# Kernel tuning notes

Hardware: AMD Instinct MI355X
Metric: run time of the kernel (lower is better)

## Reference

```python
import jax, jax.numpy as jnp
import numpy as np

N_CHARS, EMB, HID, SEQ = 256, 512, 2048, 4096

def setup_inputs() -> dict:
    key = jax.random.key(0)
    ks = jax.random.split(key, 13)
    s = lambda k, shape: jax.random.normal(k, shape, dtype=jnp.float32) * 0.02
    return {
        "input_seq": jax.random.randint(ks[0], (SEQ,), 0, N_CHARS, dtype=jnp.int32),
        "emb_table": s(ks[1], (N_CHARS, EMB)),
        "Wf": s(ks[2], (HID, EMB + HID)), "bf": s(ks[3], (HID,)),
        "Wi": s(ks[4], (HID, EMB + HID)), "bi": s(ks[5], (HID,)),
        "Wo": s(ks[6], (HID, EMB + HID)), "bo": s(ks[7], (HID,)),
        "Wc": s(ks[8], (HID, EMB + HID)), "bc": s(ks[9], (HID,)),
        "Wy": s(ks[10], (N_CHARS, HID)), "by": s(ks[11], (N_CHARS,)),
    }

def reference(input_seq, emb_table, Wf, bf, Wi, bi, Wo, bo, Wc, bc, Wy, by):
    E = emb_table.shape[1]
    embs = emb_table[input_seq]  # [T, E]
    # Split each gate Linear on concat([emb, h]) into input and recurrent parts.
    # Input contributions for all timesteps as one GEMM per gate: [T, H]
    xf = embs @ Wf[:, :E].T + bf
    xi = embs @ Wi[:, :E].T + bi
    xo = embs @ Wo[:, :E].T + bo
    xc = embs @ Wc[:, :E].T + bc
    Wfh, Wih, Woh, Wch = Wf[:, E:], Wi[:, E:], Wo[:, E:], Wc[:, E:]

    def step(carry, xs):
        h, c = carry
        xf_t, xi_t, xo_t, xc_t = xs
        ft = jax.nn.sigmoid(xf_t + Wfh @ h)
        it = jax.nn.sigmoid(xi_t + Wih @ h)
        tct = jnp.tanh(xc_t + Wch @ h)
        c_new = ft * c + it * tct
        ot = jax.nn.sigmoid(xo_t + Woh @ h)
        h_new = ot * jnp.tanh(c_new)
        o = Wy @ h_new + by
        return (h_new, c_new), o

    h0 = jnp.zeros((Wf.shape[0],), dtype=embs.dtype)
    c0 = jnp.zeros((Wf.shape[0],), dtype=embs.dtype)
    (h, c), outs = jax.lax.scan(step, (h0, c0), (xf, xi, xo, xc))
    return outs, h, c
```

## Files before the change

kernel.cpp:

```cpp
#include <hip/hip_runtime.h>
#include <hip/hip_fp16.h>

#define SEQL 4096
#define EMBD 512
#define HIDD 2048
#define NCH  256
#define WCOL 2560

typedef _Float16 half8_t __attribute__((ext_vector_type(8)));
typedef _Float16 half2_t __attribute__((ext_vector_type(2)));
typedef float    float4_t __attribute__((ext_vector_type(4)));

#if __has_builtin(__builtin_amdgcn_fdot2)
__device__ __forceinline__ float fdot2u(unsigned a, unsigned b, float c) {
  return __builtin_amdgcn_fdot2(__builtin_bit_cast(half2_t, a),
                                __builtin_bit_cast(half2_t, b), c, false);
}
#else
__device__ __forceinline__ float fdot2u(unsigned a, unsigned b, float c) {
  half2_t ha = __builtin_bit_cast(half2_t, a), hb = __builtin_bit_cast(half2_t, b);
  return c + (float)ha.x * (float)hb.x + (float)ha.y * (float)hb.y;
}
#endif

__device__ __forceinline__ float sigm_f(float x)  { return 1.f / (1.f + __expf(-x)); }
__device__ __forceinline__ float tanh_f(float x)  { return 1.f - 2.f / (__expf(2.f * x) + 1.f); }

__global__ void prep_kernel(const int* __restrict__ seq, const float* __restrict__ emb,
                            const float* __restrict__ Wf, const float* __restrict__ Wi,
                            const float* __restrict__ Wo, const float* __restrict__ Wc,
                            const float* __restrict__ Wy,
                            _Float16* __restrict__ emb16, _Float16* __restrict__ Wst16,
                            _Float16* __restrict__ Wy16, unsigned* __restrict__ hstage)
{
  const long nEmb = (long)SEQL * EMBD;
  const long nWst = (long)4 * HIDD * EMBD;
  const long nWy  = (long)NCH * HIDD;
  const long nHs  = 2 * HIDD;
  const long total = nEmb + nWst + nWy + nHs;
  long stride = (long)gridDim.x * blockDim.x;
  for (long i = (long)blockIdx.x * blockDim.x + threadIdx.x; i < total; i += stride) {
    if (i < nEmb) {
      long t = i >> 9, e = i & 511;
      emb16[i] = (_Float16)emb[(long)seq[t] * EMBD + e];
    } else if (i < nEmb + nWst) {
      long j = i - nEmb;
      long row = j >> 9, k = j & 511;
      long r = row >> 11, jr = row & 2047;
      const float* W = (r == 0) ? Wf : (r == 1) ? Wi : (r == 2) ? Wo : Wc;
      Wst16[j] = (_Float16)W[jr * WCOL + k];
    } else if (i < nEmb + nWst + nWy) {
      long j = i - nEmb - nWst;
      Wy16[j] = (_Float16)Wy[j];
    } else {
      hstage[i - nEmb - nWst - nWy] = 0u;
    }
  }
}

template<int K, int MODE>
__global__ __launch_bounds__(256) void gemm_bt(const _Float16* __restrict__ A,
                                               const _Float16* __restrict__ B,
                                               _Float16* __restrict__ C16,
                                               float* __restrict__ Cf,
                                               const float* __restrict__ bias, int N)
{
  __shared__ _Float16 At[128 * 32];
  __shared__ _Float16 Bt[128 * 32];
  const int tid = threadIdx.x;
  const int w = tid >> 6, lane = tid & 63;
  const int wm = w >> 1, wn = w & 1;
  const int lr = lane & 15, kg = lane >> 4;
  const long tm = (long)blockIdx.y * 128;
  const long tn = (long)blockIdx.x * 128;

  float4_t acc[4][4];
#pragma unroll
  for (int a = 0; a < 4; a++)
#pragma unroll
    for (int b = 0; b < 4; b++) acc[a][b] = (float4_t)0.f;

  for (int kt = 0; kt < K; kt += 32) {
    __syncthreads();
#pragma unroll
    for (int s = 0; s < 2; s++) {
      int l = s * 256 + tid;
      int row = l >> 2, ks = (l & 3) * 8;
      *(uint4*)&At[row * 32 + ks] = *(const uint4*)&A[(tm + row) * (long)K + kt + ks];
      *(uint4*)&Bt[row * 32 + ks] = *(const uint4*)&B[(tn + row) * (long)K + kt + ks];
    }
    __syncthreads();
    half8_t af[4], bf[4];
#pragma unroll
    for (int mi = 0; mi < 4; mi++) af[mi] = *(const half8_t*)&At[(wm * 64 + mi * 16 + lr) * 32 + kg * 8];
#pragma unroll
    for (int ni = 0; ni < 4; ni++) bf[ni] = *(const half8_t*)&Bt[(wn * 64 + ni * 16 + lr) * 32 + kg * 8];
#pragma unroll
    for (int mi = 0; mi < 4; mi++)
#pragma unroll
      for (int ni = 0; ni < 4; ni++)
        acc[mi][ni] = __builtin_amdgcn_mfma_f32_16x16x32_f16(af[mi], bf[ni], acc[mi][ni], 0, 0, 0);
  }

#pragma unroll
  for (int mi = 0; mi < 4; mi++)
#pragma unroll
    for (int ni = 0; ni < 4; ni++)
#pragma unroll
      for (int i = 0; i < 4; i++) {
        long gm = tm + wm * 64 + mi * 16 + kg * 4 + i;
        long gn = tn + wn * 64 + ni * 16 + lr;
        float v = acc[mi][ni][i];
        if (MODE == 0) C16[gm * (long)N + gn] = (_Float16)v;
        else           Cf[gm * (long)N + gn] = v + bias[gn];
      }
}

__global__ __launch_bounds__(512) void lstm_seq(
    const _Float16* __restrict__ xq,
    const float* __restrict__ Wf, const float* __restrict__ Wi,
    const float* __restrict__ Wo, const float* __restrict__ Wc,
    const float* __restrict__ bfp, const float* __restrict__ bip,
    const float* __restrict__ bop, const float* __restrict__ bcp,
    unsigned* __restrict__ hstage,
    _Float16* __restrict__ H16,
    float* __restrict__ out)
{
  __shared__ unsigned hbuf[HIDD / 2];
  __shared__ float gl[32];

  const int tid  = threadIdx.x;
  const int wave = tid >> 6, lane = tid & 63;
  const int rw   = lane >> 4, hsub = lane & 15;
  const int row_local = wave * 4 + rw;
  const int r  = row_local >> 3;
  const int jj = row_local & 7;
  const int g  = blockIdx.x;
  const int jg = g * 8 + jj;

  const float* Wsel = (r == 0) ? Wf : (r == 1) ? Wi : (r == 2) ? Wo : Wc;
  const float* bsel = (r == 0) ? bfp : (r == 1) ? bip : (r == 2) ? bop : bcp;
  const float* wrow = Wsel + (long)jg * WCOL + EMBD;

  uint2 wreg[32];
#pragma unroll
  for (int it = 0; it < 32; ++it) {
    const float4 wv = *(const float4*)(wrow + it * 64 + hsub * 4);
    half2_t lo = { (_Float16)wv.x, (_Float16)wv.y };
    half2_t hi = { (_Float16)wv.z, (_Float16)wv.w };
    wreg[it].x = __builtin_bit_cast(unsigned, lo);
    wreg[it].y = __builtin_bit_cast(unsigned, hi);
  }
  const float bias = (hsub == 0) ? bsel[jg] : 0.f;

  float c = 0.f;

  for (int t = 0; t < SEQL; ++t) {
    float xv = 0.f;
    if (hsub == 0) xv = (float)xq[(long)t * 8192 + r * HIDD + g * 8 + jj];

    if (t == 0) {
      hbuf[tid * 2] = 0u; hbuf[tid * 2 + 1] = 0u;
    } else {
      const int base = (t & 1) * HIDD + tid * 4;
      const unsigned tg = (unsigned)t;
      unsigned v0, v1, v2, v3; int guard = 0;
      for (;;) {
        v0 = __hip_atomic_load(&hstage[base + 0], __ATOMIC_RELAXED, __HIP_MEMORY_SCOPE_AGENT);
        v1 = __hip_atomic_load(&hstage[base + 1], __ATOMIC_RELAXED, __HIP_MEMORY_SCOPE_AGENT);
        v2 = __hip_atomic_load(&hstage[base + 2], __ATOMIC_RELAXED, __HIP_MEMORY_SCOPE_AGENT);
        v3 = __hip_atomic_load(&hstage[base + 3], __ATOMIC_RELAXED, __HIP_MEMORY_SCOPE_AGENT);
        if ((v0 >> 16) == tg && (v1 >> 16) == tg && (v2 >> 16) == tg && (v3 >> 16) == tg) break;
        if (++guard > (1 << 24)) break;
      }
      hbuf[tid * 2]     = (v0 & 0xffffu) | (v1 << 16);
      hbuf[tid * 2 + 1] = (v2 & 0xffffu) | (v3 << 16);
    }
    __syncthreads();

    float a0 = 0.f, a1 = 0.f, a2 = 0.f, a3 = 0.f;
#pragma unroll
    for (int it = 0; it < 32; ++it) {
      const uint2 hv = *(const uint2*)&hbuf[it * 32 + hsub * 2];
      if (it & 1) { a2 = fdot2u(wreg[it].x, hv.x, a2); a3 = fdot2u(wreg[it].y, hv.y, a3); }
      else        { a0 = fdot2u(wreg[it].x, hv.x, a0); a1 = fdot2u(wreg[it].y, hv.y, a1); }
    }
    float s = (a0 + a1) + (a2 + a3);
    s += __shfl_xor(s, 1, 64);
    s += __shfl_xor(s, 2, 64);
    s += __shfl_xor(s, 4, 64);
    s += __shfl_xor(s, 8, 64);

    if (hsub == 0) {
      const float pre = s + xv + bias;
      gl[row_local] = (r == 3) ? tanh_f(pre) : sigm_f(pre);
    }
    __syncthreads();

    if (tid < 8) {
      const float f  = gl[tid];
      const float ii = gl[8 + tid];
      const float o  = gl[16 + tid];
      const float cg = gl[24 + tid];
      c = f * c + ii * cg;
      const float h = o * tanh_f(c);
      const _Float16 hh = (_Float16)h;
      H16[(long)t * HIDD + g * 8 + tid] = hh;
      const unsigned pk = (unsigned)__builtin_bit_cast(unsigned short, hh) | ((unsigned)(t + 1) << 16);
      __hip_atomic_store(&hstage[((t + 1) & 1) * HIDD + g * 8 + tid], pk,
                         __ATOMIC_RELAXED, __HIP_MEMORY_SCOPE_AGENT);
      if (t == SEQL - 1) {
        out[(long)SEQL * NCH + g * 8 + tid] = h;
        out[(long)SEQL * NCH + HIDD + g * 8 + tid] = c;
      }
    }
  }
}

extern "C" void kernel_launch(void* const* d_in, const int* in_sizes, int n_in,
                              void* d_out, int out_size, void* d_ws, size_t ws_size,
                              hipStream_t stream) {
  const int*   seq = (const int*)d_in[0];
  const float* emb = (const float*)d_in[1];
  const float* Wf  = (const float*)d_in[2];
  const float* bf_ = (const float*)d_in[3];
  const float* Wi  = (const float*)d_in[4];
  const float* bi_ = (const float*)d_in[5];
  const float* Wo  = (const float*)d_in[6];
  const float* bo_ = (const float*)d_in[7];
  const float* Wc  = (const float*)d_in[8];
  const float* bc_ = (const float*)d_in[9];
  const float* Wy  = (const float*)d_in[10];
  const float* by  = (const float*)d_in[11];
  float* out = (float*)d_out;

  char* ws = (char*)d_ws;
  _Float16* xq     = (_Float16*)(ws);
  _Float16* emb16  = (_Float16*)(ws + (64ll << 20));
  _Float16* Wst16  = (_Float16*)(ws + (68ll << 20));
  _Float16* Wy16   = (_Float16*)(ws + (76ll << 20));
  _Float16* H16    = (_Float16*)(ws + (77ll << 20));
  unsigned* hstage = (unsigned*)(ws + (93ll << 20));

  prep_kernel<<<2048, 256, 0, stream>>>(seq, emb, Wf, Wi, Wo, Wc, Wy,
                                        emb16, Wst16, Wy16, hstage);

  dim3 g1(8192 / 128, 4096 / 128);
  gemm_bt<EMBD, 0><<<g1, 256, 0, stream>>>(emb16, Wst16, xq, nullptr, nullptr, 8192);

  lstm_seq<<<256, 512, 0, stream>>>(xq, Wf, Wi, Wo, Wc, bf_, bi_, bo_, bc_,
                                    hstage, H16, out);

  dim3 g2(NCH / 128, 4096 / 128);
  gemm_bt<HIDD, 1><<<g2, 256, 0, stream>>>(H16, Wy16, nullptr, out, by, NCH);
}
```

Before: 10.39 ms.

## Replace per-element tagged h handoff with per-block records and a single flag

The recurrent state exchange between blocks changes from tagging every 16-bit hidden value with the step number inside a 32-bit word to one 128-byte record per block. Each record holds that block's 8 fp16 hidden values plus a step flag written with a release store. Readers now poll only the flag, with half the threads and an s_sleep between polls, then load the 16 bytes of data. The aim is to cut polling traffic and spin pressure on the per-step cross-block barrier. In exchange, the data loads after the flag are relaxed rather than acquire, which weakens the ordering guarantee, and the sleep can add wake-up latency on the critical path.

```diff
diff --git a/kernel.cpp b/kernel.cpp
--- a/kernel.cpp
+++ b/kernel.cpp
@@ -31,13 +31,13 @@
                             const float* __restrict__ Wo, const float* __restrict__ Wc,
                             const float* __restrict__ Wy,
                             _Float16* __restrict__ emb16, _Float16* __restrict__ Wst16,
-                            _Float16* __restrict__ Wy16, unsigned* __restrict__ hstage)
+                            _Float16* __restrict__ Wy16, unsigned* __restrict__ hx)
 {
   const long nEmb = (long)SEQL * EMBD;
   const long nWst = (long)4 * HIDD * EMBD;
   const long nWy  = (long)NCH * HIDD;
-  const long nHs  = 2 * HIDD;
-  const long total = nEmb + nWst + nWy + nHs;
+  const long nHx  = 2 * 256 * 32;
+  const long total = nEmb + nWst + nWy + nHx;
   long stride = (long)gridDim.x * blockDim.x;
   for (long i = (long)blockIdx.x * blockDim.x + threadIdx.x; i < total; i += stride) {
     if (i < nEmb) {
@@ -53,7 +53,7 @@
       long j = i - nEmb - nWst;
       Wy16[j] = (_Float16)Wy[j];
     } else {
-      hstage[i - nEmb - nWst - nWy] = 0u;
+      hx[i - nEmb - nWst - nWy] = 0u;
     }
   }
 }
@@ -122,7 +122,7 @@
     const float* __restrict__ Wo, const float* __restrict__ Wc,
     const float* __restrict__ bfp, const float* __restrict__ bip,
     const float* __restrict__ bop, const float* __restrict__ bcp,
-    unsigned* __restrict__ hstage,
+    unsigned* __restrict__ hx,
     _Float16* __restrict__ H16,
     float* __restrict__ out)
 {
@@ -160,21 +160,26 @@
     if (hsub == 0) xv = (float)xq[(long)t * 8192 + r * HIDD + g * 8 + jj];
 
     if (t == 0) {
-      hbuf[tid * 2] = 0u; hbuf[tid * 2 + 1] = 0u;
-    } else {
-      const int base = (t & 1) * HIDD + tid * 4;
+      if (tid < 256) {
+        hbuf[tid * 4 + 0] = 0u; hbuf[tid * 4 + 1] = 0u;
+        hbuf[tid * 4 + 2] = 0u; hbuf[tid * 4 + 3] = 0u;
+      }
+    } else if (tid < 256) {
+      unsigned* rec = hx + (long)(t & 1) * 8192 + tid * 32;
       const unsigned tg = (unsigned)t;
-      unsigned v0, v1, v2, v3; int guard = 0;
+      int guard = 0;
       for (;;) {
-        v0 = __hip_atomic_load(&hstage[base + 0], __ATOMIC_RELAXED, __HIP_MEMORY_SCOPE_AGENT);
-        v1 = __hip_atomic_load(&hstage[base + 1], __ATOMIC_RELAXED, __HIP_MEMORY_SCOPE_AGENT);
-        v2 = __hip_atomic_load(&hstage[base + 2], __ATOMIC_RELAXED, __HIP_MEMORY_SCOPE_AGENT);
-        v3 = __hip_atomic_load(&hstage[base + 3], __ATOMIC_RELAXED, __HIP_MEMORY_SCOPE_AGENT);
-        if ((v0 >> 16) == tg && (v1 >> 16) == tg && (v2 >> 16) == tg && (v3 >> 16) == tg) break;
-        if (++guard > (1 << 24)) break;
-      }
-      hbuf[tid * 2]     = (v0 & 0xffffu) | (v1 << 16);
-      hbuf[tid * 2 + 1] = (v2 & 0xffffu) | (v3 << 16);
+        unsigned v = __hip_atomic_load(rec + 4, __ATOMIC_RELAXED, __HIP_MEMORY_SCOPE_AGENT);
+        if (v == tg) break;
+        __builtin_amdgcn_s_sleep(1);
+        if (++guard > (1 << 20)) break;
+      }
+      unsigned d0 = __hip_atomic_load(rec + 0, __ATOMIC_RELAXED, __HIP_MEMORY_SCOPE_AGENT);
+      unsigned d1 = __hip_atomic_load(rec + 1, __ATOMIC_RELAXED, __HIP_MEMORY_SCOPE_AGENT);
+      unsigned d2 = __hip_atomic_load(rec + 2, __ATOMIC_RELAXED, __HIP_MEMORY_SCOPE_AGENT);
+      unsigned d3 = __hip_atomic_load(rec + 3, __ATOMIC_RELAXED, __HIP_MEMORY_SCOPE_AGENT);
+      hbuf[tid * 4 + 0] = d0; hbuf[tid * 4 + 1] = d1;
+      hbuf[tid * 4 + 2] = d2; hbuf[tid * 4 + 3] = d3;
     }
     __syncthreads();
 
@@ -205,10 +210,14 @@
       c = f * c + ii * cg;
       const float h = o * tanh_f(c);
       const _Float16 hh = (_Float16)h;
+      unsigned* recn = hx + (long)((t + 1) & 1) * 8192 + g * 32;
+      __hip_atomic_store((unsigned short*)recn + tid,
+                         __builtin_bit_cast(unsigned short, hh),
+                         __ATOMIC_RELAXED, __HIP_MEMORY_SCOPE_AGENT);
+      if (tid == 0)
+        __hip_atomic_store(recn + 4, (unsigned)(t + 1),
+                           __ATOMIC_RELEASE, __HIP_MEMORY_SCOPE_AGENT);
       H16[(long)t * HIDD + g * 8 + tid] = hh;
-      const unsigned pk = (unsigned)__builtin_bit_cast(unsigned short, hh) | ((unsigned)(t + 1) << 16);
-      __hip_atomic_store(&hstage[((t + 1) & 1) * HIDD + g * 8 + tid], pk,
-                         __ATOMIC_RELAXED, __HIP_MEMORY_SCOPE_AGENT);
       if (t == SEQL - 1) {
         out[(long)SEQL * NCH + g * 8 + tid] = h;
         out[(long)SEQL * NCH + HIDD + g * 8 + tid] = c;
@@ -240,16 +249,16 @@
   _Float16* Wst16  = (_Float16*)(ws + (68ll << 20));
   _Float16* Wy16   = (_Float16*)(ws + (76ll << 20));
   _Float16* H16    = (_Float16*)(ws + (77ll << 20));
-  unsigned* hstage = (unsigned*)(ws + (93ll << 20));
+  unsigned* hx     = (unsigned*)(ws + (93ll << 20));
 
   prep_kernel<<<2048, 256, 0, stream>>>(seq, emb, Wf, Wi, Wo, Wc, Wy,
-                                        emb16, Wst16, Wy16, hstage);
+                                        emb16, Wst16, Wy16, hx);
 
   dim3 g1(8192 / 128, 4096 / 128);
   gemm_bt<EMBD, 0><<<g1, 256, 0, stream>>>(emb16, Wst16, xq, nullptr, nullptr, 8192);
 
   lstm_seq<<<256, 512, 0, stream>>>(xq, Wf, Wi, Wo, Wc, bf_, bi_, bo_, bc_,
-                                    hstage, H16, out);
+                                    hx, H16, out);
 
   dim3 g2(NCH / 128, 4096 / 128);
   gemm_bt<HIDD, 1><<<g2, 256, 0, stream>>>(H16, Wy16, nullptr, out, by, NCH);
```

New measurement: 29.43 ms. 2.83x slower.
